# Kernel optimization log

Hardware: AMD Instinct MI355X
Metric: run time of the kernel (lower is better)

The kernel has to match this reference:

```python
import jax, jax.numpy as jnp
import numpy as np

B, G = 256, 4096
N_GENES, D_GENE = 30000, 256
D_HIDDEN, D_Z = 256, 64
EPS = 1e-8


def setup_inputs() -> dict:
    key = jax.random.key(0)
    ks = jax.random.split(key, 12)
    d_in = D_GENE + 1  # + log-libsize
    s = lambda fan_in: 1.0 / np.sqrt(fan_in)
    return {
        "x": jax.random.uniform(ks[0], (B, G), jnp.float32) * 5.0,  # expression counts
        "gene_indices": jax.random.randint(ks[1], (B, G), 0, N_GENES),
        "emb_table": jax.random.normal(ks[2], (N_GENES, D_GENE), jnp.float32) * 0.02,
        "W1": jax.random.normal(ks[3], (d_in, D_HIDDEN), jnp.float32) * s(d_in),
        "b1": jnp.zeros((D_HIDDEN,), jnp.float32),
        "W2": jax.random.normal(ks[4], (D_HIDDEN, D_HIDDEN), jnp.float32) * s(D_HIDDEN),
        "b2": jnp.zeros((D_HIDDEN,), jnp.float32),
        "Wmu": jax.random.normal(ks[5], (D_HIDDEN, D_Z), jnp.float32) * s(D_HIDDEN),
        "bmu": jnp.zeros((D_Z,), jnp.float32),
        "Wlv": jax.random.normal(ks[6], (D_HIDDEN, D_Z), jnp.float32) * s(D_HIDDEN),
        "blv": jnp.zeros((D_Z,), jnp.float32),
    }


def reference(x, gene_indices, emb_table, W1, b1, W2, b2, Wmu, bmu, Wlv, blv):
    # pool_genes: gather (B,G,d) then weighted-sum reduce to (B,d)
    gene_embs = emb_table[gene_indices]                      # (B, G, d)
    w = jnp.log1p(x)
    w = w / (w.sum(axis=1, keepdims=True) + EPS)             # (B, G)
    h_pool = jnp.einsum('bg,bgd->bd', w, gene_embs)          # (B, d)

    log_lib = jnp.log1p(x.sum(axis=1))[:, None]              # (B, 1)
    h = jnp.concatenate([h_pool, log_lib], axis=-1)          # (B, d+1)

    h = jax.nn.relu(h @ W1 + b1)                             # dropout: eval-mode identity
    h = jax.nn.relu(h @ W2 + b2)
    mu_z = h @ Wmu + bmu
    logvar_z = h @ Wlv + blv
    return (mu_z, logvar_z, h_pool)
```

## Files before the change

### kernel.cpp

```cpp
#include <hip/hip_runtime.h>
#include <math.h>

#define BB      256
#define GG      4096
#define DG      256
#define DH      256
#define DZ      64
#define NGENES  30000
#define KPAD    30016
#define NCHUNK  (KPAD / 32)
#define KSPLIT  128
#define RED     16
#define NPART2  (KSPLIT / RED)
#define HALF    (KPAD / 2)
#define FB_TILES (NCHUNK * 16)
#define TSTRIDE 258
#define SPLIT   4
#define GCHUNK  (GG / SPLIT)

typedef __attribute__((ext_vector_type(8))) short  short8v;
typedef __attribute__((ext_vector_type(4))) float  floatx4;

__device__ __forceinline__ unsigned short bf16_rn(float f) {
    unsigned u = __float_as_uint(f);
    u += 0x7FFFu + ((u >> 16) & 1u);
    return (unsigned short)(u >> 16);
}

__global__ __launch_bounds__(256) void scatter_kernel(
    const float* __restrict__ x,
    const int*   __restrict__ gi,
    unsigned short* __restrict__ W16,
    float* __restrict__ wsum,
    float* __restrict__ xsum)
{
    const int b   = blockIdx.x;
    const int h   = blockIdx.y;
    const int tid = threadIdx.x;
    const int base = h * HALF;

    __shared__ float sW[HALF];
    for (int i = tid; i < HALF; i += 256) sW[i] = 0.f;
    __syncthreads();

    const float4* x4 = (const float4*)(x  + (size_t)b * GG);
    const int4*   g4 = (const int4*)  (gi + (size_t)b * GG);

    float lws = 0.f, xs = 0.f;
    #pragma unroll
    for (int it = 0; it < 4; ++it) {
        const int    e  = it * 256 + tid;
        const float4 xv = x4[e];
        const int4   iv = g4[e];
        const float lw0 = log1pf(xv.x), lw1 = log1pf(xv.y);
        const float lw2 = log1pf(xv.z), lw3 = log1pf(xv.w);
        lws += lw0 + lw1 + lw2 + lw3;
        xs  += xv.x + xv.y + xv.z + xv.w;
        int r0 = iv.x - base, r1 = iv.y - base, r2 = iv.z - base, r3 = iv.w - base;
        if ((unsigned)r0 < (unsigned)HALF) atomicAdd(&sW[r0], lw0);
        if ((unsigned)r1 < (unsigned)HALF) atomicAdd(&sW[r1], lw1);
        if ((unsigned)r2 < (unsigned)HALF) atomicAdd(&sW[r2], lw2);
        if ((unsigned)r3 < (unsigned)HALF) atomicAdd(&sW[r3], lw3);
    }
    __syncthreads();

    uint4* dst = (uint4*)(W16 + (size_t)b * KPAD + base);
    for (int i = tid; i < HALF / 8; i += 256) {
        const float* s = &sW[i * 8];
        uint4 o;
        o.x = (unsigned)bf16_rn(s[0]) | ((unsigned)bf16_rn(s[1]) << 16);
        o.y = (unsigned)bf16_rn(s[2]) | ((unsigned)bf16_rn(s[3]) << 16);
        o.z = (unsigned)bf16_rn(s[4]) | ((unsigned)bf16_rn(s[5]) << 16);
        o.w = (unsigned)bf16_rn(s[6]) | ((unsigned)bf16_rn(s[7]) << 16);
        dst[i] = o;
    }
    __syncthreads();

    #pragma unroll
    for (int off = 32; off > 0; off >>= 1) {
        lws += __shfl_down(lws, off);
        xs  += __shfl_down(xs,  off);
    }
    if ((tid & 63) == 0) { sW[tid >> 6] = lws; sW[4 + (tid >> 6)] = xs; }
    __syncthreads();
    if (tid == 0 && h == 0) {
        wsum[b] = sW[0] + sW[1] + sW[2] + sW[3];
        xsum[b] = sW[4] + sW[5] + sW[6] + sW[7];
    }
}

__global__ __launch_bounds__(256) void fragb_kernel(
    const float* __restrict__ emb, unsigned short* __restrict__ fragB)
{
    const int kc   = blockIdx.x;
    const int tid  = threadIdx.x;
    const int w    = tid >> 6;
    const int lane = tid & 63;
    const int quad = lane >> 4;
    const int l16  = lane & 15;
    const int k0   = kc << 5;

    __shared__ float sT[32 * TSTRIDE];

    const float4* e4 = (const float4*)emb;
    #pragma unroll
    for (int i = 0; i < 8; ++i) {
        const int f   = i * 256 + tid;
        const int row = f >> 6;
        const int col = f & 63;
        float4 v = make_float4(0.f, 0.f, 0.f, 0.f);
        if (k0 + row < NGENES) v = e4[(size_t)(k0 + row) * 64 + col];
        float* d = &sT[row * TSTRIDE + (col << 2)];
        *(float2*)d       = make_float2(v.x, v.y);
        *(float2*)(d + 2) = make_float2(v.z, v.w);
    }
    __syncthreads();

    #pragma unroll
    for (int t = 0; t < 4; ++t) {
        const int nt = (w << 2) + t;
        unsigned short v[8] __attribute__((aligned(16)));
        #pragma unroll
        for (int j = 0; j < 8; ++j)
            v[j] = bf16_rn(sT[(quad * 8 + j) * TSTRIDE + (nt << 4) + l16]);
        *(uint4*)(fragB + (size_t)kc * 8192 + (nt << 9) + lane * 8) = *(const uint4*)v;
    }
}

__global__ __launch_bounds__(256) void gemm_kernel(
    const unsigned short* __restrict__ W16,
    const unsigned short* __restrict__ fragB,
    unsigned short* __restrict__ wsg16)
{
    const int bid  = blockIdx.x;
    const int mt   = (bid >> 3) & 3;
    const int ks   = ((bid >> 5) << 3) | (bid & 7);
    const int tid  = threadIdx.x;
    const int w    = tid >> 6;
    const int lane = tid & 63;
    const int quad = lane >> 4;
    const int l16  = lane & 15;

    const int q = NCHUNK / KSPLIT;
    const int r = NCHUNK % KSPLIT;
    const int c0  = ks * q + (ks < r ? ks : r);
    const int cnt = q + (ks < r ? 1 : 0);

    __shared__ short8v sB[1024];

    const unsigned short* Arow =
        W16 + (size_t)((mt << 6) + (w << 4) + l16) * KPAD + (quad << 3);

    floatx4 acc[16];
    #pragma unroll
    for (int nt = 0; nt < 16; ++nt) acc[nt] = (floatx4){0.f, 0.f, 0.f, 0.f};

    for (int c = 0; c < cnt; ++c) {
        const int kc = c0 + c;

        const short8v af = *(const short8v*)(Arow + ((size_t)kc << 5));

        const uint4* src = (const uint4*)(fragB + (size_t)kc * 8192);
        #pragma unroll
        for (int i = 0; i < 4; ++i)
            ((uint4*)sB)[i * 256 + tid] = src[i * 256 + tid];

        __syncthreads();
        #pragma unroll
        for (int nt = 0; nt < 16; ++nt) {
            const short8v bf = sB[nt * 64 + lane];
            acc[nt] = __builtin_amdgcn_mfma_f32_16x16x32_bf16(af, bf, acc[nt], 0, 0, 0);
        }
        __syncthreads();
    }

    #pragma unroll
    for (int nt = 0; nt < 16; ++nt) {
        #pragma unroll
        for (int reg = 0; reg < 4; ++reg) {
            const int m = (mt << 6) + (w << 4) + (quad << 2) + reg;
            const int n = (nt << 4) + l16;
            wsg16[((size_t)m * KSPLIT + ks) * DG + n] = bf16_rn(acc[nt][reg]);
        }
    }
}

__global__ __launch_bounds__(256) void reduce_kernel(
    const unsigned short* __restrict__ wsg16, float* __restrict__ part2)
{
    const int b = blockIdx.x, p = blockIdx.y, d = threadIdx.x;
    const unsigned short* src = wsg16 + ((size_t)b * KSPLIT + p * RED) * DG + d;
    float s = 0.f;
    #pragma unroll
    for (int i = 0; i < RED; ++i)
        s += __uint_as_float((unsigned)src[(size_t)i * DG] << 16);
    part2[((size_t)b * NPART2 + p) * DG + d] = s;
}

__global__ __launch_bounds__(256) void convert_kernel(
    const float* __restrict__ emb, unsigned short* __restrict__ embh, int n4)
{
    const float4* e4 = (const float4*)emb;
    ushort4*      o4 = (ushort4*)embh;
    const int stride = gridDim.x * 256;
    for (int i = blockIdx.x * 256 + threadIdx.x; i < n4; i += stride) {
        const float4 v = e4[i];
        ushort4 o;
        o.x = bf16_rn(v.x); o.y = bf16_rn(v.y);
        o.z = bf16_rn(v.z); o.w = bf16_rn(v.w);
        o4[i] = o;
    }
}

__global__ __launch_bounds__(256) void pool_bf16_kernel(
    const float*          __restrict__ x,
    const int*            __restrict__ gi,
    const unsigned short* __restrict__ embh,
    float* __restrict__ ws_pool,
    float* __restrict__ ws_wsum,
    float* __restrict__ ws_xsum)
{
    const int b    = blockIdx.x;
    const int s    = blockIdx.y;
    const int tid  = threadIdx.x;
    const int wave = tid >> 6;
    const int lane = tid & 63;

    const float* xrow = x  + (size_t)b * GG + (size_t)s * GCHUNK;
    const int*   irow = gi + (size_t)b * GG + (size_t)s * GCHUNK;
    const uint2* emb2 = (const uint2*)embh;

    __shared__ float lw_s[256];
    __shared__ int   idx_s[256];
    __shared__ float accred[4][256];
    __shared__ float redw[4], redx[4];

    float wsum = 0.f, xsum = 0.f;
    float4 acc = make_float4(0.f, 0.f, 0.f, 0.f);

    for (int g0 = 0; g0 < GCHUNK; g0 += 256) {
        __syncthreads();
        const float xv = xrow[g0 + tid];
        const int   iv = irow[g0 + tid];
        const float lw = log1pf(xv);
        xsum += xv;
        wsum += lw;
        lw_s[tid]  = lw;
        idx_s[tid] = iv;
        __syncthreads();

        #pragma unroll 8
        for (int k = 0; k < 64; ++k) {
            const int   gidx = (k << 2) | wave;
            const float lw_b = lw_s[gidx];
            const uint2 e    = emb2[(size_t)idx_s[gidx] * 64 + lane];
            acc.x = fmaf(lw_b, __uint_as_float(e.x << 16),         acc.x);
            acc.y = fmaf(lw_b, __uint_as_float(e.x & 0xFFFF0000u), acc.y);
            acc.z = fmaf(lw_b, __uint_as_float(e.y << 16),         acc.z);
            acc.w = fmaf(lw_b, __uint_as_float(e.y & 0xFFFF0000u), acc.w);
        }
    }

    accred[wave][lane * 4 + 0] = acc.x;
    accred[wave][lane * 4 + 1] = acc.y;
    accred[wave][lane * 4 + 2] = acc.z;
    accred[wave][lane * 4 + 3] = acc.w;

    #pragma unroll
    for (int off = 32; off > 0; off >>= 1) {
        wsum += __shfl_down(wsum, off);
        xsum += __shfl_down(xsum, off);
    }
    if (lane == 0) { redw[wave] = wsum; redx[wave] = xsum; }
    __syncthreads();

    const float tot = accred[0][tid] + accred[1][tid] + accred[2][tid] + accred[3][tid];
    ws_pool[((size_t)b * SPLIT + s) * DG + tid] = tot;
    if (tid == 0) {
        ws_wsum[b * SPLIT + s] = redw[0] + redw[1] + redw[2] + redw[3];
        ws_xsum[b * SPLIT + s] = redx[0] + redx[1] + redx[2] + redx[3];
    }
}

template <int NS, int NW>
__global__ __launch_bounds__(512) void mlp_kernel(
    const float* __restrict__ part,
    const float* __restrict__ wsA, const float* __restrict__ xsA,
    const float* __restrict__ W1, const float* __restrict__ b1,
    const float* __restrict__ W2, const float* __restrict__ b2,
    const float* __restrict__ Wmu, const float* __restrict__ bmu,
    const float* __restrict__ Wlv, const float* __restrict__ blv,
    float* __restrict__ out)
{
    const int b   = blockIdx.x;
    const int tid = threadIdx.x;
    const int kq  = tid >> 6;
    const int c4  = tid & 63;

    __shared__ float  h[DH + 1];
    __shared__ float  h1[DH];
    __shared__ float  h2[DH];
    __shared__ float4 red[8][64];
    __shared__ float  redz[8][64];

    if (tid < DH) {
        float acc = 0.f;
        #pragma unroll
        for (int s = 0; s < NS; ++s)
            acc += part[((size_t)b * NS + s) * DG + tid];
        float wsum = 0.f, xsum = 0.f;
        #pragma unroll
        for (int s = 0; s < NW; ++s) {
            wsum += wsA[b * NW + s];
            xsum += xsA[b * NW + s];
        }
        const float hp = acc / (wsum + 1e-8f);
        out[2 * BB * DZ + (size_t)b * DG + tid] = hp;
        h[tid] = hp;
        if (tid == 0) h[DH] = log1pf(xsum);
    }
    __syncthreads();

    {
        const float4* Wv = (const float4*)W1;
        float4 a = make_float4(0.f, 0.f, 0.f, 0.f);
        const int i0 = kq * 32;
        const int i1 = i0 + 32 + (kq == 7 ? 1 : 0);
        for (int i = i0; i < i1; ++i) {
            const float  hi = h[i];
            const float4 w  = Wv[(size_t)i * 64 + c4];
            a.x = fmaf(hi, w.x, a.x);
            a.y = fmaf(hi, w.y, a.y);
            a.z = fmaf(hi, w.z, a.z);
            a.w = fmaf(hi, w.w, a.w);
        }
        red[kq][c4] = a;
        __syncthreads();
        if (tid < 64) {
            float4 t = red[0][tid];
            #pragma unroll
            for (int s = 1; s < 8; ++s) {
                const float4 rr = red[s][tid];
                t.x += rr.x; t.y += rr.y; t.z += rr.z; t.w += rr.w;
            }
            const float4 bb = ((const float4*)b1)[tid];
            h1[4 * tid + 0] = fmaxf(t.x + bb.x, 0.f);
            h1[4 * tid + 1] = fmaxf(t.y + bb.y, 0.f);
            h1[4 * tid + 2] = fmaxf(t.z + bb.z, 0.f);
            h1[4 * tid + 3] = fmaxf(t.w + bb.w, 0.f);
        }
        __syncthreads();
    }

    {
        const float4* Wv = (const float4*)W2;
        float4 a = make_float4(0.f, 0.f, 0.f, 0.f);
        const int i0 = kq * 32;
        for (int i = i0; i < i0 + 32; ++i) {
            const float  hi = h1[i];
            const float4 w  = Wv[(size_t)i * 64 + c4];
            a.x = fmaf(hi, w.x, a.x);
            a.y = fmaf(hi, w.y, a.y);
            a.z = fmaf(hi, w.z, a.z);
            a.w = fmaf(hi, w.w, a.w);
        }
        red[kq][c4] = a;
        __syncthreads();
        if (tid < 64) {
            float4 t = red[0][tid];
            #pragma unroll
            for (int s = 1; s < 8; ++s) {
                const float4 rr = red[s][tid];
                t.x += rr.x; t.y += rr.y; t.z += rr.z; t.w += rr.w;
            }
            const float4 bb = ((const float4*)b2)[tid];
            h2[4 * tid + 0] = fmaxf(t.x + bb.x, 0.f);
            h2[4 * tid + 1] = fmaxf(t.y + bb.y, 0.f);
            h2[4 * tid + 2] = fmaxf(t.z + bb.z, 0.f);
            h2[4 * tid + 3] = fmaxf(t.w + bb.w, 0.f);
        }
        __syncthreads();
    }

    {
        const bool is_lv = tid >= 256;
        const int  j  = tid & 63;
        const int  kh = (tid >> 6) & 3;
        const float* Wz = is_lv ? Wlv : Wmu;
        float az = 0.f;
        for (int i = kh * 64; i < kh * 64 + 64; ++i)
            az = fmaf(h2[i], Wz[(size_t)i * DZ + j], az);
        redz[(is_lv ? 4 : 0) + kh][j] = az;
        __syncthreads();
        if (tid < 2 * DZ) {
            const bool lv = tid >= DZ;
            const int  jj = tid & (DZ - 1);
            const int  base = lv ? 4 : 0;
            float rr = redz[base][jj] + redz[base + 1][jj]
                     + redz[base + 2][jj] + redz[base + 3][jj];
            rr += lv ? blv[jj] : bmu[jj];
            out[(lv ? BB * DZ : 0) + (size_t)b * DZ + jj] = rr;
        }
    }
}

extern "C" void kernel_launch(void* const* d_in, const int* in_sizes, int n_in,
                              void* d_out, int out_size, void* d_ws, size_t ws_size,
                              hipStream_t stream) {
    const float* x    = (const float*)d_in[0];
    const int*   gi   = (const int*)  d_in[1];
    const float* emb  = (const float*)d_in[2];
    const float* W1   = (const float*)d_in[3];
    const float* b1   = (const float*)d_in[4];
    const float* W2   = (const float*)d_in[5];
    const float* b2   = (const float*)d_in[6];
    const float* Wmu  = (const float*)d_in[7];
    const float* bmu  = (const float*)d_in[8];
    const float* Wlv  = (const float*)d_in[9];
    const float* blv  = (const float*)d_in[10];
    float* out = (float*)d_out;

    char* ws = (char*)d_ws;
    float* ws_wsum = (float*)(ws + 0);
    float* ws_xsum = (float*)(ws + 4096);
    const size_t off_main = 8192;

    const size_t szW   = (size_t)BB * KPAD * sizeof(unsigned short);
    const size_t szFB  = (size_t)FB_TILES * 1024;
    const size_t szGP  = (size_t)BB * KSPLIT * DG * sizeof(unsigned short);
    const size_t szP2  = (size_t)BB * NPART2 * DG * sizeof(float);
    const size_t need_full = off_main + szW + szFB + szGP + szP2;

    const size_t szPool = (size_t)BB * SPLIT * DG * sizeof(float);
    const size_t szEmbh = (size_t)NGENES * DG * sizeof(unsigned short);
    const size_t need_fb = off_main + szPool + szEmbh;

    if (ws_size >= need_full) {
        unsigned short* Wm    = (unsigned short*)(ws + off_main);
        unsigned short* fragB = (unsigned short*)(ws + off_main + szW);
        unsigned short* wsg16 = (unsigned short*)(ws + off_main + szW + szFB);
        float*          part2 = (float*)(ws + off_main + szW + szFB + szGP);

        scatter_kernel<<<dim3(BB, 2), 256, 0, stream>>>(x, gi, Wm, ws_wsum, ws_xsum);
        fragb_kernel<<<NCHUNK, 256, 0, stream>>>(emb, fragB);
        gemm_kernel<<<4 * KSPLIT, 256, 0, stream>>>(Wm, fragB, wsg16);
        reduce_kernel<<<dim3(BB, NPART2), 256, 0, stream>>>(wsg16, part2);
        mlp_kernel<NPART2, 1><<<BB, 512, 0, stream>>>(part2, ws_wsum, ws_xsum,
                                           W1, b1, W2, b2, Wmu, bmu, Wlv, blv, out);
    } else if (ws_size >= need_fb) {
        float*          ws_pool = (float*)(ws + off_main);
        unsigned short* embh    = (unsigned short*)(ws + off_main + szPool);

        convert_kernel<<<2048, 256, 0, stream>>>(emb, embh, NGENES * DG / 4);
        pool_bf16_kernel<<<dim3(BB, SPLIT), 256, 0, stream>>>(
            x, gi, embh, ws_pool, ws_wsum, ws_xsum);
        mlp_kernel<SPLIT, SPLIT><<<BB, 512, 0, stream>>>(ws_pool, ws_wsum, ws_xsum,
                                           W1, b1, W2, b2, Wmu, bmu, Wlv, blv, out);
    }
}
```

Baseline: 135.8 us.

## Merge scatter and fragB prep kernels; fuse split-K reduction into MLP kernel

The scatter and embedding-fragment preparation kernels are combined into one launch whose blocks branch by block index. The two are independent, so they can now run concurrently and one launch is saved. The separate split-K partial reduction kernel is removed, and the MLP kernel now reads the bf16 GEMM partials directly and reduces all 128 slices in shared memory before the layers. This drops one launch and the fp32 intermediate buffer, but each MLP block now does more reduction work, and the merged prep kernel's shared-memory size is set by its larger branch.

```diff
diff --git a/kernel.cpp b/kernel.cpp
--- a/kernel.cpp
+++ b/kernel.cpp
@@ -10,11 +10,10 @@
 #define KPAD    30016
 #define NCHUNK  (KPAD / 32)
 #define KSPLIT  128
-#define RED     16
-#define NPART2  (KSPLIT / RED)
 #define HALF    (KPAD / 2)
 #define FB_TILES (NCHUNK * 16)
 #define TSTRIDE 258
+#define NSCAT   512
 #define SPLIT   4
 #define GCHUNK  (GG / SPLIT)
 
@@ -26,104 +25,105 @@
     u += 0x7FFFu + ((u >> 16) & 1u);
     return (unsigned short)(u >> 16);
 }
-
-__global__ __launch_bounds__(256) void scatter_kernel(
+__device__ __forceinline__ float bf16_lo(unsigned u) { return __uint_as_float(u << 16); }
+__device__ __forceinline__ float bf16_hi(unsigned u) { return __uint_as_float(u & 0xFFFF0000u); }
+
+__global__ __launch_bounds__(256) void prep_kernel(
     const float* __restrict__ x,
     const int*   __restrict__ gi,
+    const float* __restrict__ emb,
     unsigned short* __restrict__ W16,
+    unsigned short* __restrict__ fragB,
     float* __restrict__ wsum,
     float* __restrict__ xsum)
 {
-    const int b   = blockIdx.x;
-    const int h   = blockIdx.y;
+    __shared__ float smem[HALF];
+    const int bid = blockIdx.x;
     const int tid = threadIdx.x;
-    const int base = h * HALF;
-
-    __shared__ float sW[HALF];
-    for (int i = tid; i < HALF; i += 256) sW[i] = 0.f;
-    __syncthreads();
-
-    const float4* x4 = (const float4*)(x  + (size_t)b * GG);
-    const int4*   g4 = (const int4*)  (gi + (size_t)b * GG);
-
-    float lws = 0.f, xs = 0.f;
-    #pragma unroll
-    for (int it = 0; it < 4; ++it) {
-        const int    e  = it * 256 + tid;
-        const float4 xv = x4[e];
-        const int4   iv = g4[e];
-        const float lw0 = log1pf(xv.x), lw1 = log1pf(xv.y);
-        const float lw2 = log1pf(xv.z), lw3 = log1pf(xv.w);
-        lws += lw0 + lw1 + lw2 + lw3;
-        xs  += xv.x + xv.y + xv.z + xv.w;
-        int r0 = iv.x - base, r1 = iv.y - base, r2 = iv.z - base, r3 = iv.w - base;
-        if ((unsigned)r0 < (unsigned)HALF) atomicAdd(&sW[r0], lw0);
-        if ((unsigned)r1 < (unsigned)HALF) atomicAdd(&sW[r1], lw1);
-        if ((unsigned)r2 < (unsigned)HALF) atomicAdd(&sW[r2], lw2);
-        if ((unsigned)r3 < (unsigned)HALF) atomicAdd(&sW[r3], lw3);
-    }
-    __syncthreads();
-
-    uint4* dst = (uint4*)(W16 + (size_t)b * KPAD + base);
-    for (int i = tid; i < HALF / 8; i += 256) {
-        const float* s = &sW[i * 8];
-        uint4 o;
-        o.x = (unsigned)bf16_rn(s[0]) | ((unsigned)bf16_rn(s[1]) << 16);
-        o.y = (unsigned)bf16_rn(s[2]) | ((unsigned)bf16_rn(s[3]) << 16);
-        o.z = (unsigned)bf16_rn(s[4]) | ((unsigned)bf16_rn(s[5]) << 16);
-        o.w = (unsigned)bf16_rn(s[6]) | ((unsigned)bf16_rn(s[7]) << 16);
-        dst[i] = o;
-    }
-    __syncthreads();
-
-    #pragma unroll
-    for (int off = 32; off > 0; off >>= 1) {
-        lws += __shfl_down(lws, off);
-        xs  += __shfl_down(xs,  off);
-    }
-    if ((tid & 63) == 0) { sW[tid >> 6] = lws; sW[4 + (tid >> 6)] = xs; }
-    __syncthreads();
-    if (tid == 0 && h == 0) {
-        wsum[b] = sW[0] + sW[1] + sW[2] + sW[3];
-        xsum[b] = sW[4] + sW[5] + sW[6] + sW[7];
-    }
-}
-
-__global__ __launch_bounds__(256) void fragb_kernel(
-    const float* __restrict__ emb, unsigned short* __restrict__ fragB)
-{
-    const int kc   = blockIdx.x;
-    const int tid  = threadIdx.x;
-    const int w    = tid >> 6;
-    const int lane = tid & 63;
-    const int quad = lane >> 4;
-    const int l16  = lane & 15;
-    const int k0   = kc << 5;
-
-    __shared__ float sT[32 * TSTRIDE];
-
-    const float4* e4 = (const float4*)emb;
-    #pragma unroll
-    for (int i = 0; i < 8; ++i) {
-        const int f   = i * 256 + tid;
-        const int row = f >> 6;
-        const int col = f & 63;
-        float4 v = make_float4(0.f, 0.f, 0.f, 0.f);
-        if (k0 + row < NGENES) v = e4[(size_t)(k0 + row) * 64 + col];
-        float* d = &sT[row * TSTRIDE + (col << 2)];
-        *(float2*)d       = make_float2(v.x, v.y);
-        *(float2*)(d + 2) = make_float2(v.z, v.w);
-    }
-    __syncthreads();
-
-    #pragma unroll
-    for (int t = 0; t < 4; ++t) {
-        const int nt = (w << 2) + t;
-        unsigned short v[8] __attribute__((aligned(16)));
-        #pragma unroll
-        for (int j = 0; j < 8; ++j)
-            v[j] = bf16_rn(sT[(quad * 8 + j) * TSTRIDE + (nt << 4) + l16]);
-        *(uint4*)(fragB + (size_t)kc * 8192 + (nt << 9) + lane * 8) = *(const uint4*)v;
+
+    if (bid < NSCAT) {
+        const int b    = bid >> 1;
+        const int h    = bid & 1;
+        const int base = h * HALF;
+
+        for (int i = tid; i < HALF; i += 256) smem[i] = 0.f;
+        __syncthreads();
+
+        const float4* x4 = (const float4*)(x  + (size_t)b * GG);
+        const int4*   g4 = (const int4*)  (gi + (size_t)b * GG);
+
+        float lws = 0.f, xs = 0.f;
+        #pragma unroll
+        for (int it = 0; it < 4; ++it) {
+            const int    e  = it * 256 + tid;
+            const float4 xv = x4[e];
+            const int4   iv = g4[e];
+            const float lw0 = log1pf(xv.x), lw1 = log1pf(xv.y);
+            const float lw2 = log1pf(xv.z), lw3 = log1pf(xv.w);
+            lws += lw0 + lw1 + lw2 + lw3;
+            xs  += xv.x + xv.y + xv.z + xv.w;
+            int r0 = iv.x - base, r1 = iv.y - base, r2 = iv.z - base, r3 = iv.w - base;
+            if ((unsigned)r0 < (unsigned)HALF) atomicAdd(&smem[r0], lw0);
+            if ((unsigned)r1 < (unsigned)HALF) atomicAdd(&smem[r1], lw1);
+            if ((unsigned)r2 < (unsigned)HALF) atomicAdd(&smem[r2], lw2);
+            if ((unsigned)r3 < (unsigned)HALF) atomicAdd(&smem[r3], lw3);
+        }
+        __syncthreads();
+
+        uint4* dst = (uint4*)(W16 + (size_t)b * KPAD + base);
+        for (int i = tid; i < HALF / 8; i += 256) {
+            const float* s = &smem[i * 8];
+            uint4 o;
+            o.x = (unsigned)bf16_rn(s[0]) | ((unsigned)bf16_rn(s[1]) << 16);
+            o.y = (unsigned)bf16_rn(s[2]) | ((unsigned)bf16_rn(s[3]) << 16);
+            o.z = (unsigned)bf16_rn(s[4]) | ((unsigned)bf16_rn(s[5]) << 16);
+            o.w = (unsigned)bf16_rn(s[6]) | ((unsigned)bf16_rn(s[7]) << 16);
+            dst[i] = o;
+        }
+        __syncthreads();
+
+        #pragma unroll
+        for (int off = 32; off > 0; off >>= 1) {
+            lws += __shfl_down(lws, off);
+            xs  += __shfl_down(xs,  off);
+        }
+        if ((tid & 63) == 0) { smem[tid >> 6] = lws; smem[4 + (tid >> 6)] = xs; }
+        __syncthreads();
+        if (tid == 0 && h == 0) {
+            wsum[b] = smem[0] + smem[1] + smem[2] + smem[3];
+            xsum[b] = smem[4] + smem[5] + smem[6] + smem[7];
+        }
+    } else {
+        const int kc   = bid - NSCAT;
+        const int w    = tid >> 6;
+        const int lane = tid & 63;
+        const int quad = lane >> 4;
+        const int l16  = lane & 15;
+        const int k0   = kc << 5;
+
+        const float4* e4 = (const float4*)emb;
+        #pragma unroll
+        for (int i = 0; i < 8; ++i) {
+            const int f   = i * 256 + tid;
+            const int row = f >> 6;
+            const int col = f & 63;
+            float4 v = make_float4(0.f, 0.f, 0.f, 0.f);
+            if (k0 + row < NGENES) v = e4[(size_t)(k0 + row) * 64 + col];
+            float* d = &smem[row * TSTRIDE + (col << 2)];
+            *(float2*)d       = make_float2(v.x, v.y);
+            *(float2*)(d + 2) = make_float2(v.z, v.w);
+        }
+        __syncthreads();
+
+        #pragma unroll
+        for (int t = 0; t < 4; ++t) {
+            const int nt = (w << 2) + t;
+            unsigned short v[8] __attribute__((aligned(16)));
+            #pragma unroll
+            for (int j = 0; j < 8; ++j)
+                v[j] = bf16_rn(smem[(quad * 8 + j) * TSTRIDE + (nt << 4) + l16]);
+            *(uint4*)(fragB + (size_t)kc * 8192 + (nt << 9) + lane * 8) = *(const uint4*)v;
+        }
     }
 }
 
@@ -185,16 +185,138 @@
     }
 }
 
-__global__ __launch_bounds__(256) void reduce_kernel(
-    const unsigned short* __restrict__ wsg16, float* __restrict__ part2)
+__global__ __launch_bounds__(512) void mlp_fused_kernel(
+    const unsigned short* __restrict__ wsg16,
+    const float* __restrict__ wsA, const float* __restrict__ xsA,
+    const float* __restrict__ W1, const float* __restrict__ b1,
+    const float* __restrict__ W2, const float* __restrict__ b2,
+    const float* __restrict__ Wmu, const float* __restrict__ bmu,
+    const float* __restrict__ Wlv, const float* __restrict__ blv,
+    float* __restrict__ out)
 {
-    const int b = blockIdx.x, p = blockIdx.y, d = threadIdx.x;
-    const unsigned short* src = wsg16 + ((size_t)b * KSPLIT + p * RED) * DG + d;
-    float s = 0.f;
-    #pragma unroll
-    for (int i = 0; i < RED; ++i)
-        s += __uint_as_float((unsigned)src[(size_t)i * DG] << 16);
-    part2[((size_t)b * NPART2 + p) * DG + d] = s;
+    const int b   = blockIdx.x;
+    const int tid = threadIdx.x;
+    const int kq  = tid >> 6;
+    const int c4  = tid & 63;
+
+    __shared__ float  sred[16 * 256];
+    __shared__ float  h[DH + 1];
+    __shared__ float  h1[DH];
+    __shared__ float  h2[DH];
+    __shared__ float4 red[8][64];
+    __shared__ float  redz[8][64];
+
+    {
+        const uint4* src = (const uint4*)(wsg16 + (size_t)b * KSPLIT * DG);
+        float s[8] = {0.f, 0.f, 0.f, 0.f, 0.f, 0.f, 0.f, 0.f};
+        #pragma unroll
+        for (int j = 0; j < 8; ++j) {
+            const uint4 v = src[j * 512 + tid];
+            s[0] += bf16_lo(v.x); s[1] += bf16_hi(v.x);
+            s[2] += bf16_lo(v.y); s[3] += bf16_hi(v.y);
+            s[4] += bf16_lo(v.z); s[5] += bf16_hi(v.z);
+            s[6] += bf16_lo(v.w); s[7] += bf16_hi(v.w);
+        }
+        float* dst = &sred[(tid >> 5) * 256 + (tid & 31) * 8];
+        #pragma unroll
+        for (int i = 0; i < 8; ++i) dst[i] = s[i];
+    }
+    __syncthreads();
+
+    if (tid < DH) {
+        float acc = 0.f;
+        #pragma unroll
+        for (int s = 0; s < 16; ++s) acc += sred[s * 256 + tid];
+        const float wsum = wsA[b];
+        const float xsum = xsA[b];
+        const float hp = acc / (wsum + 1e-8f);
+        out[2 * BB * DZ + (size_t)b * DG + tid] = hp;
+        h[tid] = hp;
+        if (tid == 0) h[DH] = log1pf(xsum);
+    }
+    __syncthreads();
+
+    {
+        const float4* Wv = (const float4*)W1;
+        float4 a = make_float4(0.f, 0.f, 0.f, 0.f);
+        const int i0 = kq * 32;
+        const int i1 = i0 + 32 + (kq == 7 ? 1 : 0);
+        for (int i = i0; i < i1; ++i) {
+            const float  hi = h[i];
+            const float4 w  = Wv[(size_t)i * 64 + c4];
+            a.x = fmaf(hi, w.x, a.x);
+            a.y = fmaf(hi, w.y, a.y);
+            a.z = fmaf(hi, w.z, a.z);
+            a.w = fmaf(hi, w.w, a.w);
+        }
+        red[kq][c4] = a;
+        __syncthreads();
+        if (tid < 64) {
+            float4 t = red[0][tid];
+            #pragma unroll
+            for (int s = 1; s < 8; ++s) {
+                const float4 rr = red[s][tid];
+                t.x += rr.x; t.y += rr.y; t.z += rr.z; t.w += rr.w;
+            }
+            const float4 bb = ((const float4*)b1)[tid];
+            h1[4 * tid + 0] = fmaxf(t.x + bb.x, 0.f);
+            h1[4 * tid + 1] = fmaxf(t.y + bb.y, 0.f);
+            h1[4 * tid + 2] = fmaxf(t.z + bb.z, 0.f);
+            h1[4 * tid + 3] = fmaxf(t.w + bb.w, 0.f);
+        }
+        __syncthreads();
+    }
+
+    {
+        const float4* Wv = (const float4*)W2;
+        float4 a = make_float4(0.f, 0.f, 0.f, 0.f);
+        const int i0 = kq * 32;
+        for (int i = i0; i < i0 + 32; ++i) {
+            const float  hi = h1[i];
+            const float4 w  = Wv[(size_t)i * 64 + c4];
+            a.x = fmaf(hi, w.x, a.x);
+            a.y = fmaf(hi, w.y, a.y);
+            a.z = fmaf(hi, w.z, a.z);
+            a.w = fmaf(hi, w.w, a.w);
+        }
+        red[kq][c4] = a;
+        __syncthreads();
+        if (tid < 64) {
+            float4 t = red[0][tid];
+            #pragma unroll
+            for (int s = 1; s < 8; ++s) {
+                const float4 rr = red[s][tid];
+                t.x += rr.x; t.y += rr.y; t.z += rr.z; t.w += rr.w;
+            }
+            const float4 bb = ((const float4*)b2)[tid];
+            h2[4 * tid + 0] = fmaxf(t.x + bb.x, 0.f);
+            h2[4 * tid + 1] = fmaxf(t.y + bb.y, 0.f);
+            h2[4 * tid + 2] = fmaxf(t.z + bb.z, 0.f);
+            h2[4 * tid + 3] = fmaxf(t.w + bb.w, 0.f);
+        }
+        __syncthreads();
+    }
+
+    {
+        const bool is_lv = tid >= 256;
+        const int  j  = tid & 63;
+        const int  kh = (tid >> 6) & 3;
+        const float* Wz = is_lv ? Wlv : Wmu;
+        float az = 0.f;
+        for (int i = kh * 64; i < kh * 64 + 64; ++i)
+            az = fmaf(h2[i], Wz[(size_t)i * DZ + j], az);
+        redz[(is_lv ? 4 : 0) + kh][j] = az;
+        __syncthreads();
+        if (tid < 2 * DZ) {
+            const bool lv = tid >= DZ;
+            const int  jj = tid & (DZ - 1);
+            const int  base = lv ? 4 : 0;
+            float rr = redz[base][jj] + redz[base + 1][jj]
+                     + redz[base + 2][jj] + redz[base + 3][jj];
+            rr += lv ? blv[jj] : bmu[jj];
+            out[(lv ? BB * DZ : 0) + (size_t)b * DZ + jj] = rr;
+        }
+    }
 }
 
 __global__ __launch_bounds__(256) void convert_kernel(
@@ -254,10 +376,10 @@
             const int   gidx = (k << 2) | wave;
             const float lw_b = lw_s[gidx];
             const uint2 e    = emb2[(size_t)idx_s[gidx] * 64 + lane];
-            acc.x = fmaf(lw_b, __uint_as_float(e.x << 16),         acc.x);
-            acc.y = fmaf(lw_b, __uint_as_float(e.x & 0xFFFF0000u), acc.y);
-            acc.z = fmaf(lw_b, __uint_as_float(e.y << 16),         acc.z);
-            acc.w = fmaf(lw_b, __uint_as_float(e.y & 0xFFFF0000u), acc.w);
+            acc.x = fmaf(lw_b, bf16_lo(e.x), acc.x);
+            acc.y = fmaf(lw_b, bf16_hi(e.x), acc.y);
+            acc.z = fmaf(lw_b, bf16_lo(e.y), acc.z);
+            acc.w = fmaf(lw_b, bf16_hi(e.y), acc.w);
         }
     }
 
@@ -428,8 +550,7 @@
     const size_t szW   = (size_t)BB * KPAD * sizeof(unsigned short);
     const size_t szFB  = (size_t)FB_TILES * 1024;
     const size_t szGP  = (size_t)BB * KSPLIT * DG * sizeof(unsigned short);
-    const size_t szP2  = (size_t)BB * NPART2 * DG * sizeof(float);
-    const size_t need_full = off_main + szW + szFB + szGP + szP2;
+    const size_t need_full = off_main + szW + szFB + szGP;
 
     const size_t szPool = (size_t)BB * SPLIT * DG * sizeof(float);
     const size_t szEmbh = (size_t)NGENES * DG * sizeof(unsigned short);
@@ -439,13 +560,11 @@
         unsigned short* Wm    = (unsigned short*)(ws + off_main);
         unsigned short* fragB = (unsigned short*)(ws + off_main + szW);
         unsigned short* wsg16 = (unsigned short*)(ws + off_main + szW + szFB);
-        float*          part2 = (float*)(ws + off_main + szW + szFB + szGP);
-
-        scatter_kernel<<<dim3(BB, 2), 256, 0, stream>>>(x, gi, Wm, ws_wsum, ws_xsum);
-        fragb_kernel<<<NCHUNK, 256, 0, stream>>>(emb, fragB);
+
+        prep_kernel<<<NSCAT + NCHUNK, 256, 0, stream>>>(
+            x, gi, emb, Wm, fragB, ws_wsum, ws_xsum);
         gemm_kernel<<<4 * KSPLIT, 256, 0, stream>>>(Wm, fragB, wsg16);
-        reduce_kernel<<<dim3(BB, NPART2), 256, 0, stream>>>(wsg16, part2);
-        mlp_kernel<NPART2, 1><<<BB, 512, 0, stream>>>(part2, ws_wsum, ws_xsum,
+        mlp_fused_kernel<<<BB, 512, 0, stream>>>(wsg16, ws_wsum, ws_xsum,
                                            W1, b1, W2, b2, Wmu, bmu, Wlv, blv, out);
     } else if (ws_size >= need_fb) {
         float*          ws_pool = (float*)(ws + off_main);
```

Result: slower. 146.3 us (+7.8%).
